# Kernel tuning notes

Measured on AMD Instinct MI355X. Metric: run time of the kernel, lower is better.

The kernel has to match this reference:

```python
import jax, jax.numpy as jnp
import numpy as np

N, D, H, E_RAW = 100000, 128, 8, 1600000
C = D // H  # head dim = 16
NEG_SLOPE = 0.2
LN_EPS = 1e-5


def _glorot(key, shape):
    fan_in, fan_out = shape[0], shape[-1]
    lim = (6.0 / (fan_in + fan_out)) ** 0.5
    return jax.random.uniform(key, shape, jnp.float32, -lim, lim)


def setup_inputs() -> dict:
    key = jax.random.key(0)
    ks = jax.random.split(key, 16)
    inp = {
        "x": jax.random.normal(ks[0], (N, D), jnp.float32),
        "edge_index": jax.random.randint(ks[1], (2, E_RAW), 0, N, jnp.int64),
    }
    for l in range(2):
        o = 2 + 4 * l
        inp[f"Wl{l}"] = _glorot(ks[o + 0], (D, H * C))
        inp[f"Wr{l}"] = _glorot(ks[o + 1], (D, H * C))
        inp[f"att{l}"] = _glorot(ks[o + 2], (H, C))
        inp[f"b{l}"] = jnp.zeros((H * C,), jnp.float32)
        inp[f"g{l}"] = jnp.ones((D,), jnp.float32)
        inp[f"beta{l}"] = jnp.zeros((D,), jnp.float32)
    return inp


def _gatv2_layer(x, src, dst, Wl, Wr, att, b):
    # GATv2Conv: e_ij = att . leaky_relu(Wl x_j + Wr x_i); softmax over j -> i
    xl = (x @ Wl).reshape(N, H, C)  # source transform
    xr = (x @ Wr).reshape(N, H, C)  # target transform
    m = jax.nn.leaky_relu(xl[src] + xr[dst], NEG_SLOPE)  # [E,H,C]
    e = jnp.einsum("ehc,hc->eh", m, att)  # [E,H]
    emax = jax.ops.segment_max(e, dst, num_segments=N)[dst]
    ex = jnp.exp(e - emax)
    denom = jax.ops.segment_sum(ex, dst, num_segments=N)[dst]
    alpha = ex / denom  # per-destination softmax
    out = jax.ops.segment_sum(xl[src] * alpha[:, :, None], dst, num_segments=N)
    return out.reshape(N, H * C) + b


def _layernorm(x, g, beta):
    mu = jnp.mean(x, axis=-1, keepdims=True)
    var = jnp.var(x, axis=-1, keepdims=True)
    return (x - mu) * jax.lax.rsqrt(var + LN_EPS) * g + beta


def reference(x, edge_index, Wl0, Wr0, att0, b0, g0, beta0,
              Wl1, Wr1, att1, b1, g1, beta1):
    # add_self_loops=True (PyG default): every node attends to itself
    loop = jnp.arange(N, dtype=edge_index.dtype)
    src = jnp.concatenate([edge_index[0], loop])
    dst = jnp.concatenate([edge_index[1], loop])
    params = [(Wl0, Wr0, att0, b0, g0, beta0), (Wl1, Wr1, att1, b1, g1, beta1)]
    for Wl, Wr, att, b, g, beta in params:
        residual = x
        h = _gatv2_layer(x, src, dst, Wl, Wr, att, b)  # dropout is identity (eval)
        h = jax.nn.elu(h)
        x = _layernorm(h + residual, g, beta)
    return x
```

## Files before the change

kernel.cpp:

```cpp
#include <hip/hip_runtime.h>
#include <cstdint>

#define LEAKY 0.2f
#define LN_EPS 1e-5f

typedef __attribute__((ext_vector_type(8))) short short8;
typedef __attribute__((ext_vector_type(4))) float f32x4;
typedef __attribute__((ext_vector_type(2))) float f32x2;

__device__ __forceinline__ ushort bf16_rne(float x) {
    unsigned u = __float_as_uint(x);
    unsigned r = (u + 0x7fffu + ((u >> 16) & 1u)) >> 16;
    return (ushort)r;
}
__device__ __forceinline__ float bf16_to_f(ushort h) {
    return __uint_as_float(((unsigned)h) << 16);
}

__global__ void hist_kernel(const int* __restrict__ ei, int er, int etot,
                            int* __restrict__ deg) {
    int e = blockIdx.x * blockDim.x + threadIdx.x;
    if (e >= etot) return;
    int dst = (e < er) ? ei[er + e] : (e - er);
    atomicAdd(&deg[dst], 1);
}

__global__ __launch_bounds__(1024) void scanA(const int* __restrict__ deg,
                                              int* __restrict__ escan,
                                              int* __restrict__ bsum, int n) {
    __shared__ int wsum[16], wpre[16];
    const int lane = threadIdx.x & 63, wv = threadIdx.x >> 6;
    const int i = blockIdx.x * 1024 + threadIdx.x;
    int v = (i < n) ? deg[i] : 0;
    int x = v;
#pragma unroll
    for (int off = 1; off < 64; off <<= 1) {
        int y = __shfl_up(x, off, 64);
        if (lane >= off) x += y;
    }
    if (lane == 63) wsum[wv] = x;
    __syncthreads();
    if (wv == 0) {
        int s = (lane < 16) ? wsum[lane] : 0;
#pragma unroll
        for (int off = 1; off < 16; off <<= 1) {
            int y = __shfl_up(s, off, 64);
            if (lane >= off) s += y;
        }
        if (lane < 16) wpre[lane] = s;
    }
    __syncthreads();
    int excl = x - v + (wv ? wpre[wv - 1] : 0);
    if (i < n) escan[i] = excl;
    if (threadIdx.x == 1023) bsum[blockIdx.x] = wpre[15];
}

__global__ __launch_bounds__(1024) void scanB(const int* __restrict__ bsum,
                                              int* __restrict__ bpre, int nb,
                                              int* __restrict__ offs, int n) {
    __shared__ int wsum[16], wpre[16];
    const int lane = threadIdx.x & 63, wv = threadIdx.x >> 6;
    const int i = threadIdx.x;
    int v = (i < nb) ? bsum[i] : 0;
    int x = v;
#pragma unroll
    for (int off = 1; off < 64; off <<= 1) {
        int y = __shfl_up(x, off, 64);
        if (lane >= off) x += y;
    }
    if (lane == 63) wsum[wv] = x;
    __syncthreads();
    if (wv == 0) {
        int s = (lane < 16) ? wsum[lane] : 0;
#pragma unroll
        for (int off = 1; off < 16; off <<= 1) {
            int y = __shfl_up(s, off, 64);
            if (lane >= off) s += y;
        }
        if (lane < 16) wpre[lane] = s;
    }
    __syncthreads();
    if (i < nb) bpre[i] = x - v + (wv ? wpre[wv - 1] : 0);
    if (threadIdx.x == 1023) offs[n] = wpre[15];
}

__global__ void scanC(const int* __restrict__ escan, const int* __restrict__ bpre,
                      int* __restrict__ offs, int* __restrict__ woff, int n) {
    int i = blockIdx.x * 256 + threadIdx.x;
    if (i >= n) return;
    int o = escan[i] + bpre[i >> 10];
    offs[i] = o;
    woff[i] = o;
}

__global__ void fill_kernel(const int* __restrict__ ei, int er, int etot,
                            int* __restrict__ woff, int* __restrict__ colv) {
    int e = blockIdx.x * blockDim.x + threadIdx.x;
    if (e >= etot) return;
    int src, dst;
    if (e < er) { src = ei[e]; dst = ei[er + e]; }
    else        { src = dst = e - er; }
    int pos = atomicAdd(&woff[dst], 1);
    colv[pos] = src;
}

__global__ void cvt_w2(const float* __restrict__ Wl0, const float* __restrict__ Wr0,
                       const float* __restrict__ Wl1, const float* __restrict__ Wr1,
                       ushort* __restrict__ Whi, ushort* __restrict__ Wlo) {
    int t = blockIdx.x * 256 + threadIdx.x;
    int layer = t >> 15;
    int i = t & 32767;
    int colblk = i >> 11;
    int ks = (i >> 9) & 3;
    int lane = (i >> 3) & 63;
    int j = i & 7;
    int col = colblk * 16 + (lane & 15);
    int k = ks * 32 + (lane >> 4) * 8 + j;
    const float* Wl = layer ? Wl1 : Wl0;
    const float* Wr = layer ? Wr1 : Wr0;
    float v = (col < 128) ? Wl[(size_t)k * 128 + col]
                          : Wr[(size_t)k * 128 + (col - 128)];
    ushort h = bf16_rne(v);
    Whi[t] = h;
    Wlo[t] = bf16_rne(v - bf16_to_f(h));
}

__global__ __launch_bounds__(256) void gemm_mfma(
    const float* __restrict__ X,
    const ushort* __restrict__ Wfhi, const ushort* __restrict__ Wflo,
    uint* __restrict__ Olb, uint* __restrict__ Orb, int nrows) {
    __shared__ float xs[64 * 32 * 4];
    const int t = threadIdx.x;
    const int wave = t >> 6, lane = t & 63;
    const int m0 = blockIdx.x * 64;
    {
        const float4* Xv = (const float4*)X + (size_t)m0 * 32;
        float4* xsv = (float4*)xs;
#pragma unroll
        for (int i = 0; i < 8; ++i) {
            int idx = i * 256 + t;
            int row = idx >> 5, kc = idx & 31;
            float4 v = {0.f, 0.f, 0.f, 0.f};
            if (m0 + row < nrows) v = Xv[idx];
            xsv[row * 32 + (kc ^ (row & 7))] = v;
        }
    }
    __syncthreads();

    const int lrow = lane & 15;
    const int lkc = (lane >> 4) * 2;
    f32x4 acc[4][4];
#pragma unroll
    for (int mt = 0; mt < 4; ++mt)
#pragma unroll
        for (int nt = 0; nt < 4; ++nt) acc[mt][nt] = (f32x4){0.f, 0.f, 0.f, 0.f};

#pragma unroll 1
    for (int ks = 0; ks < 4; ++ks) {
        short8 ahi[4], alo[4];
#pragma unroll
        for (int mt = 0; mt < 4; ++mt) {
            const int row = mt * 16 + lrow;
            const int kc0 = ks * 8 + lkc;
            float4 v0 = ((const float4*)xs)[row * 32 + (kc0 ^ (row & 7))];
            float4 v1 = ((const float4*)xs)[row * 32 + ((kc0 + 1) ^ (row & 7))];
            float e[8];
            e[0] = v0.x; e[1] = v0.y; e[2] = v0.z; e[3] = v0.w;
            e[4] = v1.x; e[5] = v1.y; e[6] = v1.z; e[7] = v1.w;
#pragma unroll
            for (int j = 0; j < 8; ++j) {
                ushort h = (ushort)(__float_as_uint(e[j]) >> 16);
                ahi[mt][j] = (short)h;
                alo[mt][j] = (short)bf16_rne(e[j] - bf16_to_f(h));
            }
        }
#pragma unroll
        for (int nt = 0; nt < 4; ++nt) {
            size_t off = (((size_t)(wave * 4 + nt) * 4 + ks) * 64 + lane) * 8;
            short8 bhi = *(const short8*)&Wfhi[off];
            short8 blo = *(const short8*)&Wflo[off];
#pragma unroll
            for (int mt = 0; mt < 4; ++mt) {
                acc[mt][nt] = __builtin_amdgcn_mfma_f32_16x16x32_bf16(
                    alo[mt], bhi, acc[mt][nt], 0, 0, 0);
                acc[mt][nt] = __builtin_amdgcn_mfma_f32_16x16x32_bf16(
                    ahi[mt], blo, acc[mt][nt], 0, 0, 0);
                acc[mt][nt] = __builtin_amdgcn_mfma_f32_16x16x32_bf16(
                    ahi[mt], bhi, acc[mt][nt], 0, 0, 0);
            }
        }
    }
    uint* __restrict__ O = (wave < 2) ? Olb : Orb;
    const int cbase = (wave * 64) & 127;
    const int crow0 = (lane >> 4) * 4;
    const bool evn = (lane & 1) == 0;
#pragma unroll
    for (int mt = 0; mt < 4; ++mt) {
#pragma unroll
        for (int i = 0; i < 4; ++i) {
            const int row = m0 + mt * 16 + crow0 + i;
#pragma unroll
            for (int nt = 0; nt < 4; ++nt) {
                float val = acc[mt][nt][i];
                float pv = __shfl_xor(val, 1);
                uint pk = (uint)bf16_rne(val) | ((uint)bf16_rne(pv) << 16);
                if (evn && row < nrows) {
                    const int col = cbase + nt * 16 + lrow;
                    O[(size_t)row * 64 + (col >> 1)] = pk;
                }
            }
        }
    }
}

__global__ __launch_bounds__(256) void gat_agg(
    const uint* __restrict__ xl, const uint* __restrict__ xr,
    const int* __restrict__ offs, const int* __restrict__ colv,
    const float* __restrict__ att,
    const float* __restrict__ bias, const float* __restrict__ gamma,
    const float* __restrict__ beta, const float* __restrict__ resid,
    float* __restrict__ out, int nnode) {
    const int lane = threadIdx.x & 63;
    const int wave0 = blockIdx.x * 4 + (threadIdx.x >> 6);
    const int wstride = gridDim.x * 4;
    const uint* __restrict__ xlb = xl + lane;
    const f32x2 att2 = ((const f32x2*)att)[lane];
    const f32x2 b2 = ((const f32x2*)bias)[lane];
    const f32x2 g2 = ((const f32x2*)gamma)[lane];
    const f32x2 be2 = ((const f32x2*)beta)[lane];
    for (int gid = wave0; gid < nnode; gid += wstride) {
        const uint xru = __builtin_nontemporal_load(xr + (size_t)gid * 64 + lane);
        const float xrx = __uint_as_float(xru << 16);
        const float xry = __uint_as_float(xru & 0xffff0000u);
        float den = 0.f, acc0 = 0.f, acc1 = 0.f;
        int e = offs[gid];
        const int e1 = offs[gid + 1];
        for (; e + 4 <= e1; e += 4) {
            int s0 = colv[e], s1 = colv[e + 1], s2 = colv[e + 2], s3 = colv[e + 3];
            uint u0 = xlb[(size_t)s0 * 64];
            uint u1 = xlb[(size_t)s1 * 64];
            uint u2 = xlb[(size_t)s2 * 64];
            uint u3 = xlb[(size_t)s3 * 64];
            float a0x = __uint_as_float(u0 << 16), a0y = __uint_as_float(u0 & 0xffff0000u);
            float a1x = __uint_as_float(u1 << 16), a1y = __uint_as_float(u1 & 0xffff0000u);
            float a2x = __uint_as_float(u2 << 16), a2y = __uint_as_float(u2 & 0xffff0000u);
            float a3x = __uint_as_float(u3 << 16), a3y = __uint_as_float(u3 & 0xffff0000u);
            float m0x = a0x + xrx, m0y = a0y + xry;
            float m1x = a1x + xrx, m1y = a1y + xry;
            float m2x = a2x + xrx, m2y = a2y + xry;
            float m3x = a3x + xrx, m3y = a3y + xry;
            m0x = fmaxf(m0x, LEAKY * m0x); m0y = fmaxf(m0y, LEAKY * m0y);
            m1x = fmaxf(m1x, LEAKY * m1x); m1y = fmaxf(m1y, LEAKY * m1y);
            m2x = fmaxf(m2x, LEAKY * m2x); m2y = fmaxf(m2y, LEAKY * m2y);
            m3x = fmaxf(m3x, LEAKY * m3x); m3y = fmaxf(m3y, LEAKY * m3y);
            float p0 = m0x * att2.x + m0y * att2.y;
            float p1 = m1x * att2.x + m1y * att2.y;
            float p2 = m2x * att2.x + m2y * att2.y;
            float p3 = m3x * att2.x + m3y * att2.y;
            p0 += __shfl_xor(p0, 1); p0 += __shfl_xor(p0, 2); p0 += __shfl_xor(p0, 4);
            p1 += __shfl_xor(p1, 1); p1 += __shfl_xor(p1, 2); p1 += __shfl_xor(p1, 4);
            p2 += __shfl_xor(p2, 1); p2 += __shfl_xor(p2, 2); p2 += __shfl_xor(p2, 4);
            p3 += __shfl_xor(p3, 1); p3 += __shfl_xor(p3, 2); p3 += __shfl_xor(p3, 4);
            float ex0 = __expf(p0), ex1 = __expf(p1);
            float ex2 = __expf(p2), ex3 = __expf(p3);
            den += (ex0 + ex1) + (ex2 + ex3);
            acc0 += a0x * ex0 + a1x * ex1 + a2x * ex2 + a3x * ex3;
            acc1 += a0y * ex0 + a1y * ex1 + a2y * ex2 + a3y * ex3;
        }
        for (; e < e1; ++e) {
            int s0 = colv[e];
            uint u0 = xlb[(size_t)s0 * 64];
            float a0x = __uint_as_float(u0 << 16), a0y = __uint_as_float(u0 & 0xffff0000u);
            float m0x = a0x + xrx, m0y = a0y + xry;
            m0x = fmaxf(m0x, LEAKY * m0x);
            m0y = fmaxf(m0y, LEAKY * m0y);
            float p0 = m0x * att2.x + m0y * att2.y;
            p0 += __shfl_xor(p0, 1); p0 += __shfl_xor(p0, 2); p0 += __shfl_xor(p0, 4);
            float ex0 = __expf(p0);
            den += ex0;
            acc0 += a0x * ex0;
            acc1 += a0y * ex0;
        }
        float inv_den = 1.f / den;
        float v0 = acc0 * inv_den + b2.x;
        float v1 = acc1 * inv_den + b2.y;
        v0 = v0 > 0.f ? v0 : expm1f(v0);
        v1 = v1 > 0.f ? v1 : expm1f(v1);
        const f32x2 r2 = __builtin_nontemporal_load(
            (const f32x2*)resid + (size_t)gid * 64 + lane);
        float t0 = v0 + r2.x, t1 = v1 + r2.y;
        float s = t0 + t1, ss = t0 * t0 + t1 * t1;
#pragma unroll
        for (int m = 1; m < 64; m <<= 1) {
            s += __shfl_xor(s, m);
            ss += __shfl_xor(ss, m);
        }
        const float mu = s * 0.0078125f;
        const float var = ss * 0.0078125f - mu * mu;
        const float iv = rsqrtf(var + LN_EPS);
        f32x2 o;
        o.x = (t0 - mu) * iv * g2.x + be2.x;
        o.y = (t1 - mu) * iv * g2.y + be2.y;
        __builtin_nontemporal_store(o, (f32x2*)out + (size_t)gid * 64 + lane);
    }
}

extern "C" void kernel_launch(void* const* d_in, const int* in_sizes, int n_in,
                              void* d_out, int out_size, void* d_ws, size_t ws_size,
                              hipStream_t stream) {
    const float* x   = (const float*)d_in[0];
    const int*   ei  = (const int*)d_in[1];
    const float* Wl0 = (const float*)d_in[2];
    const float* Wr0 = (const float*)d_in[3];
    const float* at0 = (const float*)d_in[4];
    const float* b0  = (const float*)d_in[5];
    const float* g0  = (const float*)d_in[6];
    const float* be0 = (const float*)d_in[7];
    const float* Wl1 = (const float*)d_in[8];
    const float* Wr1 = (const float*)d_in[9];
    const float* at1 = (const float*)d_in[10];
    const float* b1  = (const float*)d_in[11];
    const float* g1  = (const float*)d_in[12];
    const float* be1 = (const float*)d_in[13];

    const int NF = in_sizes[0];
    const int n  = NF / 128;
    const int er = in_sizes[1] / 2;
    const int etot = er + n;
    const int nb = (n + 1023) / 1024;

    uint* A     = (uint*)d_ws;
    uint* B     = A + (size_t)NF / 2;
    ushort* Whi = (ushort*)(B + (size_t)NF / 2);
    ushort* Wlo = Whi + 65536;
    int* deg    = (int*)(Wlo + 65536);
    int* woff   = deg + n;
    int* offs   = woff + n;
    int* escan  = offs + (n + 1);
    int* bsum   = escan + n;
    int* bpre   = bsum + 1024;
    int* colv   = bpre + 1024;
    float* C    = (float*)d_out;

    (void)hipMemsetAsync(deg, 0, (size_t)n * sizeof(int), stream);
    hist_kernel<<<(etot + 255) / 256, 256, 0, stream>>>(ei, er, etot, deg);
    scanA<<<nb, 1024, 0, stream>>>(deg, escan, bsum, n);
    scanB<<<1, 1024, 0, stream>>>(bsum, bpre, nb, offs, n);
    scanC<<<(n + 255) / 256, 256, 0, stream>>>(escan, bpre, offs, woff, n);
    fill_kernel<<<(etot + 255) / 256, 256, 0, stream>>>(ei, er, etot, woff, colv);
    cvt_w2<<<256, 256, 0, stream>>>(Wl0, Wr0, Wl1, Wr1, Whi, Wlo);

    const int gblk = (n + 63) / 64;

    gemm_mfma<<<gblk, 256, 0, stream>>>(x, Whi, Wlo, A, B, n);
    gat_agg<<<2048, 256, 0, stream>>>(A, B, offs, colv, at0, b0, g0, be0,
                                      x, C, n);
    gemm_mfma<<<gblk, 256, 0, stream>>>(C, Whi + 32768, Wlo + 32768, A, B, n);
    gat_agg<<<2048, 256, 0, stream>>>(A, B, offs, colv, at1, b1, g1, be1,
                                      C, C, n);
}
```

Measured before the change: 527.4 us.

## Partition histogram and CSR fill atomics by destination range per XCD

The histogram and CSR fill kernels become grid-stride loops over a fixed 2048-block grid. Each block, keyed by blockIdx mod 8 (assumed to map to an XCD), handles only destinations in one eighth of the node range. The aim is to keep each deg/woff counter's atomics inside one XCD's L2 and avoid cross-die coherence traffic on the atomics. The cost is that every edge index is read eight times, once by each partition group.

```diff
diff --git a/kernel.cpp b/kernel.cpp
--- a/kernel.cpp
+++ b/kernel.cpp
@@ -17,12 +17,34 @@
     return __uint_as_float(((unsigned)h) << 16);
 }
 
-__global__ void hist_kernel(const int* __restrict__ ei, int er, int etot,
-                            int* __restrict__ deg) {
-    int e = blockIdx.x * blockDim.x + threadIdx.x;
-    if (e >= etot) return;
-    int dst = (e < er) ? ei[er + e] : (e - er);
-    atomicAdd(&deg[dst], 1);
+__global__ void hist_part(const int* __restrict__ ei, int er, int etot, int n,
+                          int* __restrict__ deg) {
+    const int xcd = blockIdx.x & 7;
+    const int lo = (int)((long long)n * xcd >> 3);
+    const int hi = (int)((long long)n * (xcd + 1) >> 3);
+    const int stride = (gridDim.x >> 3) * blockDim.x;
+    for (int e = (blockIdx.x >> 3) * blockDim.x + threadIdx.x; e < etot;
+         e += stride) {
+        int dst = (e < er) ? ei[er + e] : (e - er);
+        if (dst >= lo && dst < hi) atomicAdd(&deg[dst], 1);
+    }
+}
+
+__global__ void fill_part(const int* __restrict__ ei, int er, int etot, int n,
+                          int* __restrict__ woff, int* __restrict__ colv) {
+    const int xcd = blockIdx.x & 7;
+    const int lo = (int)((long long)n * xcd >> 3);
+    const int hi = (int)((long long)n * (xcd + 1) >> 3);
+    const int stride = (gridDim.x >> 3) * blockDim.x;
+    for (int e = (blockIdx.x >> 3) * blockDim.x + threadIdx.x; e < etot;
+         e += stride) {
+        int dst = (e < er) ? ei[er + e] : (e - er);
+        if (dst >= lo && dst < hi) {
+            int src = (e < er) ? ei[e] : dst;
+            int pos = atomicAdd(&woff[dst], 1);
+            colv[pos] = src;
+        }
+    }
 }
 
 __global__ __launch_bounds__(1024) void scanA(const int* __restrict__ deg,
@@ -91,17 +113,6 @@
     int o = escan[i] + bpre[i >> 10];
     offs[i] = o;
     woff[i] = o;
-}
-
-__global__ void fill_kernel(const int* __restrict__ ei, int er, int etot,
-                            int* __restrict__ woff, int* __restrict__ colv) {
-    int e = blockIdx.x * blockDim.x + threadIdx.x;
-    if (e >= etot) return;
-    int src, dst;
-    if (e < er) { src = ei[e]; dst = ei[er + e]; }
-    else        { src = dst = e - er; }
-    int pos = atomicAdd(&woff[dst], 1);
-    colv[pos] = src;
 }
 
 __global__ void cvt_w2(const float* __restrict__ Wl0, const float* __restrict__ Wr0,
@@ -343,11 +354,11 @@
     float* C    = (float*)d_out;
 
     (void)hipMemsetAsync(deg, 0, (size_t)n * sizeof(int), stream);
-    hist_kernel<<<(etot + 255) / 256, 256, 0, stream>>>(ei, er, etot, deg);
+    hist_part<<<2048, 256, 0, stream>>>(ei, er, etot, n, deg);
     scanA<<<nb, 1024, 0, stream>>>(deg, escan, bsum, n);
     scanB<<<1, 1024, 0, stream>>>(bsum, bpre, nb, offs, n);
     scanC<<<(n + 255) / 256, 256, 0, stream>>>(escan, bpre, offs, woff, n);
-    fill_kernel<<<(etot + 255) / 256, 256, 0, stream>>>(ei, er, etot, woff, colv);
+    fill_part<<<2048, 256, 0, stream>>>(ei, er, etot, n, woff, colv);
     cvt_w2<<<256, 256, 0, stream>>>(Wl0, Wr0, Wl1, Wr1, Whi, Wlo);
 
     const int gblk = (n + 63) / 64;
```

After: 470.5 us. 10.8% less time.
